# Kernel optimization log

Measured on AMD Instinct MI355X. Metric: run time of the kernel, lower is better.

The kernel has to match this reference:

```python
import jax, jax.numpy as jnp
import numpy as np

N_NODES = 100000
N_EDGES = 1600000
DIMS = [1, 20, 40, 60, 80, 100]  # int(k/5*qubo_size) for qubo_size=100


def setup_inputs() -> dict:
    key = jax.random.key(0)
    ks = jax.random.split(key, 16)
    inp = {
        "x": jax.random.normal(ks[0], (N_NODES, 1), dtype=jnp.float32),
        "edge_index": jax.random.randint(ks[1], (2, N_EDGES), 0, N_NODES, dtype=jnp.int64),
        "edge_weights": jax.random.uniform(ks[2], (N_EDGES,), dtype=jnp.float32),
    }
    for i in range(5):
        fan_in, fan_out = DIMS[i], DIMS[i + 1]
        scale = (2.0 / (fan_in + fan_out)) ** 0.5  # glorot-ish
        inp[f"W{i+1}"] = jax.random.normal(ks[3 + 2 * i], (fan_in, fan_out), dtype=jnp.float32) * scale
        inp[f"b{i+1}"] = jnp.zeros((fan_out,), dtype=jnp.float32)
    return inp


def reference(x, edge_index, edge_weights, W1, b1, W2, b2, W3, b3, W4, b4, W5, b5):
    n = x.shape[0]
    src, dst = edge_index[0], edge_index[1]
    # GCN symmetric normalization with self loops (fill value 1.0)
    deg = jax.ops.segment_sum(edge_weights, dst, num_segments=n) + 1.0
    dinv = jnp.where(deg > 0, deg ** -0.5, 0.0)
    norm = dinv[src] * edge_weights * dinv[dst]  # [E]
    self_norm = dinv * dinv                      # [N], self-loop weight 1

    def gcn_layer(h, W, b):
        h = h @ W  # [N, out]
        agg = jax.ops.segment_sum(h[src] * norm[:, None], dst, num_segments=n)
        agg = agg + h * self_norm[:, None]
        return agg + b

    for W, b in ((W1, b1), (W2, b2), (W3, b3), (W4, b4), (W5, b5)):
        x = gcn_layer(x, W, b)
    return jax.nn.relu(x)
```

## Files before the change

kernel.cpp:

```cpp
#include <hip/hip_runtime.h>


#define TBB 1024
#define TBK 512
#define BN 256
#define NBLK 256
#define CAP 4864
#define EPB 7
#define MAGIC 0x13572468

__device__ __forceinline__ void chains_block(
    const float* __restrict__ W1, const float* __restrict__ b1,
    const float* __restrict__ W2, const float* __restrict__ b2,
    const float* __restrict__ W3, const float* __restrict__ b3,
    const float* __restrict__ W4, const float* __restrict__ b4,
    const float* __restrict__ W5, float* __restrict__ coef,
    int* lflag, float (*A)[112], float (*Bm)[112]) {
    int t = threadIdx.x;
    if (t < 20) { A[0][t] = W1[t]; A[1][t] = b1[t]; }
    __syncthreads();
    if (t < 40) {
        for (int c = 0; c < 2; ++c) {
            float acc = 0.f;
            for (int k = 0; k < 20; ++k) acc += A[c][k] * W2[k * 40 + t];
            Bm[c][t] = acc;
        }
        Bm[2][t] = b2[t];
    }
    __syncthreads();
    if (t < 60) {
        for (int c = 0; c < 3; ++c) {
            float acc = 0.f;
            for (int k = 0; k < 40; ++k) acc += Bm[c][k] * W3[k * 60 + t];
            A[c][t] = acc;
        }
        A[3][t] = b3[t];
    }
    __syncthreads();
    if (t < 80) {
        for (int c = 0; c < 4; ++c) {
            float acc = 0.f;
            for (int k = 0; k < 60; ++k) acc += A[c][k] * W4[k * 80 + t];
            Bm[c][t] = acc;
        }
        Bm[4][t] = b4[t];
    }
    __syncthreads();
    if (t < 100) {
        int nz = 0;
        for (int c = 0; c < 5; ++c) {
            float acc = 0.f;
            for (int k = 0; k < 80; ++k) acc += Bm[c][k] * W5[k * 100 + t];
            coef[c * 100 + t] = acc;
            if (c > 0 && acc != 0.0f) nz = 1;
        }
        if (nz) atomicOr(lflag, 1);
    }
}

__global__ __launch_bounds__(TBB) void k_build(const int* __restrict__ src,
                                               const int* __restrict__ dst,
                                               const float* __restrict__ w,
                                               int* __restrict__ gcur,
                                               int* __restrict__ ready,
                                               int2* __restrict__ payload,
                                               const float* __restrict__ W1, const float* __restrict__ b1,
                                               const float* __restrict__ W2, const float* __restrict__ b2,
                                               const float* __restrict__ W3, const float* __restrict__ b3,
                                               const float* __restrict__ W4, const float* __restrict__ b4,
                                               const float* __restrict__ W5, float* __restrict__ coef,
                                               int* __restrict__ uflag,
                                               int E, int B, int chunk) {
    __shared__ int lcnt[512];
    __shared__ int lrnk[512];
    __shared__ int goff[512];
    __shared__ float chain_scratch[10][112];
    int blk = blockIdx.x, tid = threadIdx.x;
    if (blk == NBLK) {
        if (tid == 0) lcnt[0] = 0;
        __syncthreads();
        chains_block(W1, b1, W2, b2, W3, b3, W4, b4, W5, coef, &lcnt[0],
                     &chain_scratch[0], &chain_scratch[5]);
        __syncthreads();
        if (tid == 0) uflag[0] = lcnt[0] ? 0 : 1;
        return;
    }
    if (blk == 0) {
        for (int j2 = tid; j2 < B; j2 += TBB) gcur[j2] = 0;
        __syncthreads();
        if (tid == 0)
            __hip_atomic_store(ready, MAGIC, __ATOMIC_RELEASE, __HIP_MEMORY_SCOPE_AGENT);
    }
    if (tid < 512) { lcnt[tid] = 0; lrnk[tid] = 0; }
    __syncthreads();
    int e0 = blk * chunk, e1 = min(E, e0 + chunk);
    int es[EPB], ed[EPB]; float ew[EPB]; int ne = 0;
    for (int i = e0 + tid; i < e1; i += TBB) {
        es[ne] = src[i]; ed[ne] = dst[i]; ew[ne] = w[i]; ++ne;
    }
    for (int k = 0; k < ne; ++k) atomicAdd(&lcnt[ed[k] >> 8], 1);
    __syncthreads();
    if (blk != 0) {
        if (tid == 0) {
            while (__hip_atomic_load(ready, __ATOMIC_ACQUIRE, __HIP_MEMORY_SCOPE_AGENT) != MAGIC)
                __builtin_amdgcn_s_sleep(1);
        }
        __syncthreads();
    }
    if (tid < 512) {
        int c = lcnt[tid];
        if (c > 0) goff[tid] = atomicAdd(&gcur[tid], c);
    }
    __syncthreads();
    for (int k = 0; k < ne; ++k) {
        int j = ed[k] >> 8;
        int r = atomicAdd(&lrnk[j], 1);
        int slot = goff[j] + r;
        if (slot < CAP)
            payload[(size_t)j * CAP + slot] =
                make_int2(es[k] | ((ed[k] & 255) << 17), __float_as_int(ew[k]));
    }
}

__global__ __launch_bounds__(TBK) void k_bstats(const int* __restrict__ gcur,
                                                const int2* __restrict__ payload,
                                                const float* __restrict__ x,
                                                float* __restrict__ dinv,
                                                float* __restrict__ selfn,
                                                float* __restrict__ qx0,
                                                float* __restrict__ qy0, int n) {
    __shared__ float wdeg[BN];
    int j = blockIdx.x;
    int tid = threadIdx.x;
    if (tid < BN) wdeg[tid] = 0.f;
    __syncthreads();
    int len = min(gcur[j], CAP);
    const int2* row = payload + (size_t)j * CAP;
    const int4* row4 = (const int4*)row;
    int len2 = len >> 1;
    for (int i = tid; i < len2; i += TBK) {
        int4 p = row4[i];
        atomicAdd(&wdeg[(p.x >> 17) & 255], __int_as_float(p.y));
        atomicAdd(&wdeg[(p.z >> 17) & 255], __int_as_float(p.w));
    }
    if (tid == 0 && (len & 1)) {
        int2 p = row[len - 1];
        atomicAdd(&wdeg[(p.x >> 17) & 255], __int_as_float(p.y));
    }
    __syncthreads();
    if (tid < BN) {
        int v = j * BN + tid;
        if (v < n) {
            float di = rsqrtf(wdeg[tid] + 1.0f);
            dinv[v] = di;
            selfn[v] = di * di;
            qx0[v] = di * x[v];
            qy0[v] = di;
        }
    }
}

__global__ __launch_bounds__(TBK) void k_mid(const int* __restrict__ gcur,
                                             const int2* __restrict__ payload,
                                             const float* __restrict__ qxin,
                                             const float* __restrict__ qyin,
                                             const float* __restrict__ selfn,
                                             const int* __restrict__ uflag,
                                             float* __restrict__ qxout,
                                             float* __restrict__ qyout, int n) {
    __shared__ float sacc_x[BN];
    __shared__ float sacc_y[BN];
    int j = blockIdx.x;
    int tid = threadIdx.x;
    if (tid < BN) { sacc_x[tid] = 0.f; sacc_y[tid] = 0.f; }
    __syncthreads();
    const int skipy = uflag[0];
    int len = min(gcur[j], CAP);
    const int2* row = payload + (size_t)j * CAP;
    const int4* row4 = (const int4*)row;
    int len2 = len >> 1;
    for (int i = tid; i < len2; i += TBK) {
        int4 p = row4[i];
        int s1 = p.x & 0x1FFFF, s2 = p.z & 0x1FFFF;
        int ld1 = (p.x >> 17) & 255, ld2 = (p.z >> 17) & 255;
        float w1 = __int_as_float(p.y), w2 = __int_as_float(p.w);
        if (skipy) {
            float qx1 = qxin[s1], qx2 = qxin[s2];
            atomicAdd(&sacc_x[ld1], w1 * qx1);
            atomicAdd(&sacc_x[ld2], w2 * qx2);
        } else {
            float qx1 = qxin[s1], qy1 = qyin[s1];
            float qx2 = qxin[s2], qy2 = qyin[s2];
            atomicAdd(&sacc_x[ld1], w1 * qx1);
            atomicAdd(&sacc_y[ld1], w1 * qy1);
            atomicAdd(&sacc_x[ld2], w2 * qx2);
            atomicAdd(&sacc_y[ld2], w2 * qy2);
        }
    }
    if (tid == 0 && (len & 1)) {
        int2 p = row[len - 1];
        int s = p.x & 0x1FFFF, ld = (p.x >> 17) & 255;
        float wv = __int_as_float(p.y);
        atomicAdd(&sacc_x[ld], wv * qxin[s]);
        if (!skipy) atomicAdd(&sacc_y[ld], wv * qyin[s]);
    }
    __syncthreads();
    if (tid < BN) {
        int v = j * BN + tid;
        if (v < n) {
            float sf = selfn[v];
            qxout[v] = sf * (sacc_x[tid] + qxin[v]);
            if (!skipy) qyout[v] = sf * (sacc_y[tid] + qyin[v]);
        }
    }
}

__global__ __launch_bounds__(TBK) void k_last(const int* __restrict__ gcur,
                                              const int2* __restrict__ payload,
                                              const float* __restrict__ qx4,
                                              const float* __restrict__ qy1,
                                              const float* __restrict__ qy2,
                                              const float* __restrict__ qy3,
                                              const float* __restrict__ qy4,
                                              const float* __restrict__ dinv,
                                              const int* __restrict__ uflag,
                                              const float* __restrict__ coef,
                                              const float* __restrict__ b5,
                                              float4* __restrict__ out, int n) {
    __shared__ float sacc_x[BN];
    __shared__ float scoef[500];
    __shared__ float sb5[100];
    __shared__ float snode[BN * 5];
    int j = blockIdx.x;
    int tid = threadIdx.x;
    if (tid < BN) sacc_x[tid] = 0.f;
    for (int i = tid; i < 500; i += TBK) scoef[i] = coef[i];
    for (int i = tid; i < 100; i += TBK) sb5[i] = b5[i];
    __syncthreads();
    const int skipy = uflag[0];
    int len = min(gcur[j], CAP);
    const int2* row = payload + (size_t)j * CAP;
    const int4* row4 = (const int4*)row;
    int len2 = len >> 1;
    for (int i = tid; i < len2; i += TBK) {
        int4 p = row4[i];
        float qx1 = qx4[p.x & 0x1FFFF];
        float qx2 = qx4[p.z & 0x1FFFF];
        atomicAdd(&sacc_x[(p.x >> 17) & 255], __int_as_float(p.y) * qx1);
        atomicAdd(&sacc_x[(p.z >> 17) & 255], __int_as_float(p.w) * qx2);
    }
    if (tid == 0 && (len & 1)) {
        int2 p = row[len - 1];
        atomicAdd(&sacc_x[(p.x >> 17) & 255], __int_as_float(p.y) * qx4[p.x & 0x1FFFF]);
    }
    __syncthreads();
    if (tid < BN) {
        int v = j * BN + tid;
        if (v < n) {
            float dv = dinv[v];
            float inv = 1.0f / dv;
            snode[tid * 5 + 0] = dv * (sacc_x[tid] + qx4[v]);
            snode[tid * 5 + 1] = skipy ? 0.f : qy4[v] * inv;
            snode[tid * 5 + 2] = skipy ? 0.f : qy3[v] * inv;
            snode[tid * 5 + 3] = skipy ? 0.f : qy2[v] * inv;
            snode[tid * 5 + 4] = skipy ? 0.f : qy1[v] * inv;
        }
    }
    __syncthreads();
    int base_v = j * BN;
    int nv = min(BN, n - base_v);
    int total4 = nv * 25;
    for (int q = tid; q < total4; q += TBK) {
        int lv = q / 25;
        int col4 = q - lv * 25;
        int c0 = col4 * 4;
        float a5 = snode[lv * 5 + 0], u4 = snode[lv * 5 + 1], u3 = snode[lv * 5 + 2],
              u2 = snode[lv * 5 + 3], u1 = snode[lv * 5 + 4];
        float4 r;
        float* rp = (float*)&r;
#pragma unroll
        for (int kk = 0; kk < 4; ++kk) {
            int c = c0 + kk;
            rp[kk] = fmaxf(sb5[c] + a5 * scoef[c] + u4 * scoef[100 + c] + u3 * scoef[200 + c]
                           + u2 * scoef[300 + c] + u1 * scoef[400 + c], 0.f);
        }
        out[(size_t)(base_v + lv) * 25 + col4] = r;
    }
}


extern "C" void kernel_launch(void* const* d_in, const int* in_sizes, int n_in,
                              void* d_out, int out_size, void* d_ws, size_t ws_size,
                              hipStream_t stream) {
    const float* x  = (const float*)d_in[0];
    const int*   ei = (const int*)d_in[1];
    const float* w  = (const float*)d_in[2];
    const float* W1 = (const float*)d_in[3];  const float* b1 = (const float*)d_in[4];
    const float* W2 = (const float*)d_in[5];  const float* b2 = (const float*)d_in[6];
    const float* W3 = (const float*)d_in[7];  const float* b3 = (const float*)d_in[8];
    const float* W4 = (const float*)d_in[9];  const float* b4 = (const float*)d_in[10];
    const float* W5 = (const float*)d_in[11]; const float* b5 = (const float*)d_in[12];

    const int n = in_sizes[0];
    const int E = in_sizes[2];
    const int* src = ei;
    const int* dst = ei + E;

    const int B = (n + BN - 1) / BN;
    const int chunk = (E + NBLK - 1) / NBLK;

    char* ws = (char*)d_ws;
    size_t off = 0;
    auto alloc = [&](size_t bytes) -> void* {
        void* p = ws + off;
        off += (bytes + 255) & ~(size_t)255;
        return p;
    };
    int*   gcur    = (int*)alloc((size_t)B * 4);
    int*   ready   = (int*)alloc(256);
    int*   uflag   = (int*)alloc(256);
    float* dinv    = (float*)alloc((size_t)n * 4);
    float* selfn   = (float*)alloc((size_t)n * 4);
    float* coef    = (float*)alloc(512 * 4);
    int2*  payload = (int2*)alloc((size_t)B * CAP * 8);
    float* qx[5];
    float* qy[5];
    for (int i = 0; i < 5; ++i) qx[i] = (float*)alloc((size_t)n * 4);
    for (int i = 0; i < 5; ++i) qy[i] = (float*)alloc((size_t)n * 4);

    k_build<<<NBLK + 1, TBB, 0, stream>>>(src, dst, w, gcur, ready, payload,
                                          W1, b1, W2, b2, W3, b3, W4, b4, W5, coef,
                                          uflag, E, B, chunk);
    k_bstats<<<B, TBK, 0, stream>>>(gcur, payload, x, dinv, selfn, qx[0], qy[0], n);

    for (int k = 1; k < 5; ++k)
        k_mid<<<B, TBK, 0, stream>>>(gcur, payload, qx[k - 1], qy[k - 1], selfn, uflag,
                                     qx[k], qy[k], n);
    k_last<<<B, TBK, 0, stream>>>(gcur, payload, qx[4], qy[1], qy[2], qy[3], qy[4],
                                  dinv, uflag, coef, b5, (float4*)d_out, n);
}
```

Before: 206.1 us.

## Fuse all stages into one persistent kernel with grid barriers and LDS-cached bucket rows

Merges the build, degree-stats, four middle propagation passes and final output pass into a single kernel of B=391 blocks (512 threads each), synchronised by atomic grid barriers. Each block caches its destination bucket's payload row in shared memory once and reuses it across all six passes. dinv and selfn now stay in shared memory instead of global arrays. This removes six kernel launches and the repeated global payload reads. In exchange, correctness depends on all 391 blocks being co-resident: a software grid barrier without cooperative launch can deadlock if they are not. The large shared-memory footprint (about 39 KB for the row alone) also limits occupancy.

```diff
diff --git a/kernel.cpp b/kernel.cpp
--- a/kernel.cpp
+++ b/kernel.cpp
@@ -1,12 +1,10 @@
 #include <hip/hip_runtime.h>
 
 
-#define TBB 1024
 #define TBK 512
 #define BN 256
-#define NBLK 256
 #define CAP 4864
-#define EPB 7
+#define EPB 8
 #define MAGIC 0x13572468
 
 __device__ __forceinline__ void chains_block(
@@ -58,213 +56,203 @@
     }
 }
 
-__global__ __launch_bounds__(TBB) void k_build(const int* __restrict__ src,
-                                               const int* __restrict__ dst,
-                                               const float* __restrict__ w,
-                                               int* __restrict__ gcur,
-                                               int* __restrict__ ready,
-                                               int2* __restrict__ payload,
-                                               const float* __restrict__ W1, const float* __restrict__ b1,
-                                               const float* __restrict__ W2, const float* __restrict__ b2,
-                                               const float* __restrict__ W3, const float* __restrict__ b3,
-                                               const float* __restrict__ W4, const float* __restrict__ b4,
-                                               const float* __restrict__ W5, float* __restrict__ coef,
-                                               int* __restrict__ uflag,
-                                               int E, int B, int chunk) {
-    __shared__ int lcnt[512];
-    __shared__ int lrnk[512];
-    __shared__ int goff[512];
-    __shared__ float chain_scratch[10][112];
-    int blk = blockIdx.x, tid = threadIdx.x;
-    if (blk == NBLK) {
-        if (tid == 0) lcnt[0] = 0;
-        __syncthreads();
-        chains_block(W1, b1, W2, b2, W3, b3, W4, b4, W5, coef, &lcnt[0],
-                     &chain_scratch[0], &chain_scratch[5]);
-        __syncthreads();
-        if (tid == 0) uflag[0] = lcnt[0] ? 0 : 1;
-        return;
-    }
-    if (blk == 0) {
-        for (int j2 = tid; j2 < B; j2 += TBB) gcur[j2] = 0;
-        __syncthreads();
-        if (tid == 0)
-            __hip_atomic_store(ready, MAGIC, __ATOMIC_RELEASE, __HIP_MEMORY_SCOPE_AGENT);
-    }
-    if (tid < 512) { lcnt[tid] = 0; lrnk[tid] = 0; }
-    __syncthreads();
-    int e0 = blk * chunk, e1 = min(E, e0 + chunk);
-    int es[EPB], ed[EPB]; float ew[EPB]; int ne = 0;
-    for (int i = e0 + tid; i < e1; i += TBB) {
-        es[ne] = src[i]; ed[ne] = dst[i]; ew[ne] = w[i]; ++ne;
-    }
-    for (int k = 0; k < ne; ++k) atomicAdd(&lcnt[ed[k] >> 8], 1);
-    __syncthreads();
-    if (blk != 0) {
-        if (tid == 0) {
-            while (__hip_atomic_load(ready, __ATOMIC_ACQUIRE, __HIP_MEMORY_SCOPE_AGENT) != MAGIC)
-                __builtin_amdgcn_s_sleep(1);
-        }
-        __syncthreads();
-    }
-    if (tid < 512) {
-        int c = lcnt[tid];
-        if (c > 0) goff[tid] = atomicAdd(&gcur[tid], c);
-    }
-    __syncthreads();
-    for (int k = 0; k < ne; ++k) {
-        int j = ed[k] >> 8;
-        int r = atomicAdd(&lrnk[j], 1);
-        int slot = goff[j] + r;
-        if (slot < CAP)
-            payload[(size_t)j * CAP + slot] =
-                make_int2(es[k] | ((ed[k] & 255) << 17), __float_as_int(ew[k]));
-    }
-}
-
-__global__ __launch_bounds__(TBK) void k_bstats(const int* __restrict__ gcur,
-                                                const int2* __restrict__ payload,
-                                                const float* __restrict__ x,
-                                                float* __restrict__ dinv,
-                                                float* __restrict__ selfn,
-                                                float* __restrict__ qx0,
-                                                float* __restrict__ qy0, int n) {
-    __shared__ float wdeg[BN];
-    int j = blockIdx.x;
+__device__ __forceinline__ void gbar(int* bar, int target) {
+    __syncthreads();
+    if (threadIdx.x == 0) {
+        __hip_atomic_fetch_add(bar, 1, __ATOMIC_RELEASE, __HIP_MEMORY_SCOPE_AGENT);
+        while (__hip_atomic_load(bar, __ATOMIC_RELAXED, __HIP_MEMORY_SCOPE_AGENT) < target)
+            __builtin_amdgcn_s_sleep(2);
+        __builtin_amdgcn_fence(__ATOMIC_ACQUIRE, "agent");
+    }
+    __syncthreads();
+}
+
+__device__ __forceinline__ void midpass(const int4* srow, int len,
+                                        const float* qxin, const float* qyin,
+                                        float* qxout, float* qyout,
+                                        float* sacc_x, float* sacc_y,
+                                        const float* sselfn, int skipy, int n) {
     int tid = threadIdx.x;
-    if (tid < BN) wdeg[tid] = 0.f;
-    __syncthreads();
-    int len = min(gcur[j], CAP);
-    const int2* row = payload + (size_t)j * CAP;
-    const int4* row4 = (const int4*)row;
+    if (tid < BN) { sacc_x[tid] = 0.f; sacc_y[tid] = 0.f; }
+    __syncthreads();
     int len2 = len >> 1;
     for (int i = tid; i < len2; i += TBK) {
-        int4 p = row4[i];
-        atomicAdd(&wdeg[(p.x >> 17) & 255], __int_as_float(p.y));
-        atomicAdd(&wdeg[(p.z >> 17) & 255], __int_as_float(p.w));
-    }
-    if (tid == 0 && (len & 1)) {
-        int2 p = row[len - 1];
-        atomicAdd(&wdeg[(p.x >> 17) & 255], __int_as_float(p.y));
-    }
-    __syncthreads();
-    if (tid < BN) {
-        int v = j * BN + tid;
-        if (v < n) {
-            float di = rsqrtf(wdeg[tid] + 1.0f);
-            dinv[v] = di;
-            selfn[v] = di * di;
-            qx0[v] = di * x[v];
-            qy0[v] = di;
-        }
-    }
-}
-
-__global__ __launch_bounds__(TBK) void k_mid(const int* __restrict__ gcur,
-                                             const int2* __restrict__ payload,
-                                             const float* __restrict__ qxin,
-                                             const float* __restrict__ qyin,
-                                             const float* __restrict__ selfn,
-                                             const int* __restrict__ uflag,
-                                             float* __restrict__ qxout,
-                                             float* __restrict__ qyout, int n) {
-    __shared__ float sacc_x[BN];
-    __shared__ float sacc_y[BN];
-    int j = blockIdx.x;
-    int tid = threadIdx.x;
-    if (tid < BN) { sacc_x[tid] = 0.f; sacc_y[tid] = 0.f; }
-    __syncthreads();
-    const int skipy = uflag[0];
-    int len = min(gcur[j], CAP);
-    const int2* row = payload + (size_t)j * CAP;
-    const int4* row4 = (const int4*)row;
-    int len2 = len >> 1;
-    for (int i = tid; i < len2; i += TBK) {
-        int4 p = row4[i];
+        int4 p = srow[i];
         int s1 = p.x & 0x1FFFF, s2 = p.z & 0x1FFFF;
         int ld1 = (p.x >> 17) & 255, ld2 = (p.z >> 17) & 255;
         float w1 = __int_as_float(p.y), w2 = __int_as_float(p.w);
         if (skipy) {
-            float qx1 = qxin[s1], qx2 = qxin[s2];
-            atomicAdd(&sacc_x[ld1], w1 * qx1);
-            atomicAdd(&sacc_x[ld2], w2 * qx2);
+            atomicAdd(&sacc_x[ld1], w1 * qxin[s1]);
+            atomicAdd(&sacc_x[ld2], w2 * qxin[s2]);
         } else {
-            float qx1 = qxin[s1], qy1 = qyin[s1];
-            float qx2 = qxin[s2], qy2 = qyin[s2];
-            atomicAdd(&sacc_x[ld1], w1 * qx1);
-            atomicAdd(&sacc_y[ld1], w1 * qy1);
-            atomicAdd(&sacc_x[ld2], w2 * qx2);
-            atomicAdd(&sacc_y[ld2], w2 * qy2);
+            float qxa = qxin[s1], qya = qyin[s1];
+            float qxb = qxin[s2], qyb = qyin[s2];
+            atomicAdd(&sacc_x[ld1], w1 * qxa);
+            atomicAdd(&sacc_y[ld1], w1 * qya);
+            atomicAdd(&sacc_x[ld2], w2 * qxb);
+            atomicAdd(&sacc_y[ld2], w2 * qyb);
         }
     }
     if (tid == 0 && (len & 1)) {
-        int2 p = row[len - 1];
+        int4 p = srow[len2];
         int s = p.x & 0x1FFFF, ld = (p.x >> 17) & 255;
         float wv = __int_as_float(p.y);
         atomicAdd(&sacc_x[ld], wv * qxin[s]);
         if (!skipy) atomicAdd(&sacc_y[ld], wv * qyin[s]);
     }
     __syncthreads();
-    if (tid < BN) {
-        int v = j * BN + tid;
-        if (v < n) {
-            float sf = selfn[v];
-            qxout[v] = sf * (sacc_x[tid] + qxin[v]);
-            if (!skipy) qyout[v] = sf * (sacc_y[tid] + qyin[v]);
-        }
-    }
-}
-
-__global__ __launch_bounds__(TBK) void k_last(const int* __restrict__ gcur,
-                                              const int2* __restrict__ payload,
-                                              const float* __restrict__ qx4,
-                                              const float* __restrict__ qy1,
-                                              const float* __restrict__ qy2,
-                                              const float* __restrict__ qy3,
-                                              const float* __restrict__ qy4,
-                                              const float* __restrict__ dinv,
-                                              const int* __restrict__ uflag,
-                                              const float* __restrict__ coef,
-                                              const float* __restrict__ b5,
-                                              float4* __restrict__ out, int n) {
+    int v = blockIdx.x * BN + tid;
+    if (tid < BN && v < n) {
+        float sf = sselfn[tid];
+        qxout[v] = sf * (sacc_x[tid] + qxin[v]);
+        if (!skipy) qyout[v] = sf * (sacc_y[tid] + qyin[v]);
+    }
+}
+
+__global__ __launch_bounds__(TBK, 4) void k_all(
+    const int* __restrict__ src, const int* __restrict__ dst,
+    const float* __restrict__ w, const float* __restrict__ x,
+    const float* __restrict__ W1, const float* __restrict__ b1,
+    const float* __restrict__ W2, const float* __restrict__ b2,
+    const float* __restrict__ W3, const float* __restrict__ b3,
+    const float* __restrict__ W4, const float* __restrict__ b4,
+    const float* __restrict__ W5, const float* __restrict__ b5,
+    int* gcur, int* ready, int* bar, int* uflag, float* coef,
+    int2* payload,
+    float* qx0, float* qx1, float* qx2, float* qx3, float* qx4,
+    float* qy0, float* qy1, float* qy2, float* qy3, float* qy4,
+    float4* out, int n, int E, int B, int chunk) {
+    __shared__ int lcnt[512];
+    __shared__ int lrnk[512];
+    __shared__ int goff[512];
+    __shared__ int4 srow[CAP / 2];
     __shared__ float sacc_x[BN];
+    __shared__ float sacc_y[BN];
+    __shared__ float sdinv[BN];
+    __shared__ float sselfn[BN];
     __shared__ float scoef[500];
     __shared__ float sb5[100];
     __shared__ float snode[BN * 5];
-    int j = blockIdx.x;
-    int tid = threadIdx.x;
+
+    int j = blockIdx.x, tid = threadIdx.x;
+
+    lcnt[tid] = 0; lrnk[tid] = 0;
+    __syncthreads();
+    int e0 = j * chunk, e1 = min(E, e0 + chunk);
+    int es[EPB], ed[EPB]; float ew[EPB];
+#pragma unroll
+    for (int k = 0; k < EPB; ++k) {
+        int i = e0 + tid + k * TBK;
+        if (i < e1) { es[k] = src[i]; ed[k] = dst[i]; ew[k] = w[i]; }
+        else ed[k] = -1;
+    }
+#pragma unroll
+    for (int k = 0; k < EPB; ++k)
+        if (ed[k] >= 0) atomicAdd(&lcnt[ed[k] >> 8], 1);
+    __syncthreads();
+    if (j == 0) {
+        for (int q = tid; q < B; q += TBK) gcur[q] = 0;
+        if (tid == 0) bar[0] = 0;
+        __syncthreads();
+        if (tid == 0)
+            __hip_atomic_store(ready, MAGIC, __ATOMIC_RELEASE, __HIP_MEMORY_SCOPE_AGENT);
+    } else {
+        if (tid == 0) {
+            while (__hip_atomic_load(ready, __ATOMIC_RELAXED, __HIP_MEMORY_SCOPE_AGENT) != MAGIC)
+                __builtin_amdgcn_s_sleep(2);
+            __builtin_amdgcn_fence(__ATOMIC_ACQUIRE, "agent");
+        }
+        __syncthreads();
+    }
+    {
+        int c = lcnt[tid];
+        if (c > 0) goff[tid] = atomicAdd(&gcur[tid], c);
+    }
+    __syncthreads();
+#pragma unroll
+    for (int k = 0; k < EPB; ++k) {
+        if (ed[k] >= 0) {
+            int b = ed[k] >> 8;
+            int r = atomicAdd(&lrnk[b], 1);
+            int slot = goff[b] + r;
+            if (slot < CAP)
+                payload[(size_t)b * CAP + slot] =
+                    make_int2(es[k] | ((ed[k] & 255) << 17), __float_as_int(ew[k]));
+        }
+    }
+    gbar(bar, B);
+
+    int len = min(gcur[j], CAP);
+    int len2 = len >> 1;
+    int nq4 = (len + 1) >> 1;
+    const int4* row4g = (const int4*)(payload + (size_t)j * CAP);
+    for (int i = tid; i < nq4; i += TBK) srow[i] = row4g[i];
     if (tid < BN) sacc_x[tid] = 0.f;
+    __syncthreads();
+    for (int i = tid; i < len2; i += TBK) {
+        int4 p = srow[i];
+        atomicAdd(&sacc_x[(p.x >> 17) & 255], __int_as_float(p.y));
+        atomicAdd(&sacc_x[(p.z >> 17) & 255], __int_as_float(p.w));
+    }
+    if (tid == 0 && (len & 1)) {
+        int4 p = srow[len2];
+        atomicAdd(&sacc_x[(p.x >> 17) & 255], __int_as_float(p.y));
+    }
+    __syncthreads();
+    int v = j * BN + tid;
+    if (tid < BN && v < n) {
+        float di = rsqrtf(sacc_x[tid] + 1.0f);
+        sdinv[tid] = di;
+        sselfn[tid] = di * di;
+        qx0[v] = di * x[v];
+        qy0[v] = di;
+    }
+    if (j == 0) {
+        float (*A)[112]  = (float (*)[112])snode;
+        float (*Bm)[112] = (float (*)[112])(snode + 5 * 112);
+        if (tid == 0) lcnt[0] = 0;
+        __syncthreads();
+        chains_block(W1, b1, W2, b2, W3, b3, W4, b4, W5, coef, &lcnt[0], A, Bm);
+        __syncthreads();
+        if (tid == 0) uflag[0] = lcnt[0] ? 0 : 1;
+    }
+    gbar(bar, 2 * B);
+
+    const int skipy = uflag[0];
     for (int i = tid; i < 500; i += TBK) scoef[i] = coef[i];
     for (int i = tid; i < 100; i += TBK) sb5[i] = b5[i];
-    __syncthreads();
-    const int skipy = uflag[0];
-    int len = min(gcur[j], CAP);
-    const int2* row = payload + (size_t)j * CAP;
-    const int4* row4 = (const int4*)row;
-    int len2 = len >> 1;
+
+    midpass(srow, len, qx0, qy0, qx1, qy1, sacc_x, sacc_y, sselfn, skipy, n);
+    gbar(bar, 3 * B);
+    midpass(srow, len, qx1, qy1, qx2, qy2, sacc_x, sacc_y, sselfn, skipy, n);
+    gbar(bar, 4 * B);
+    midpass(srow, len, qx2, qy2, qx3, qy3, sacc_x, sacc_y, sselfn, skipy, n);
+    gbar(bar, 5 * B);
+    midpass(srow, len, qx3, qy3, qx4, qy4, sacc_x, sacc_y, sselfn, skipy, n);
+    gbar(bar, 6 * B);
+
+    if (tid < BN) sacc_x[tid] = 0.f;
+    __syncthreads();
     for (int i = tid; i < len2; i += TBK) {
-        int4 p = row4[i];
-        float qx1 = qx4[p.x & 0x1FFFF];
-        float qx2 = qx4[p.z & 0x1FFFF];
-        atomicAdd(&sacc_x[(p.x >> 17) & 255], __int_as_float(p.y) * qx1);
-        atomicAdd(&sacc_x[(p.z >> 17) & 255], __int_as_float(p.w) * qx2);
+        int4 p = srow[i];
+        float q1 = qx4[p.x & 0x1FFFF];
+        float q2 = qx4[p.z & 0x1FFFF];
+        atomicAdd(&sacc_x[(p.x >> 17) & 255], __int_as_float(p.y) * q1);
+        atomicAdd(&sacc_x[(p.z >> 17) & 255], __int_as_float(p.w) * q2);
     }
     if (tid == 0 && (len & 1)) {
-        int2 p = row[len - 1];
+        int4 p = srow[len2];
         atomicAdd(&sacc_x[(p.x >> 17) & 255], __int_as_float(p.y) * qx4[p.x & 0x1FFFF]);
     }
     __syncthreads();
-    if (tid < BN) {
-        int v = j * BN + tid;
-        if (v < n) {
-            float dv = dinv[v];
-            float inv = 1.0f / dv;
-            snode[tid * 5 + 0] = dv * (sacc_x[tid] + qx4[v]);
-            snode[tid * 5 + 1] = skipy ? 0.f : qy4[v] * inv;
-            snode[tid * 5 + 2] = skipy ? 0.f : qy3[v] * inv;
-            snode[tid * 5 + 3] = skipy ? 0.f : qy2[v] * inv;
-            snode[tid * 5 + 4] = skipy ? 0.f : qy1[v] * inv;
-        }
+    if (tid < BN && v < n) {
+        float dv = sdinv[tid];
+        float inv = 1.0f / dv;
+        snode[tid * 5 + 0] = dv * (sacc_x[tid] + qx4[v]);
+        snode[tid * 5 + 1] = skipy ? 0.f : qy4[v] * inv;
+        snode[tid * 5 + 2] = skipy ? 0.f : qy3[v] * inv;
+        snode[tid * 5 + 3] = skipy ? 0.f : qy2[v] * inv;
+        snode[tid * 5 + 4] = skipy ? 0.f : qy1[v] * inv;
     }
     __syncthreads();
     int base_v = j * BN;
@@ -307,7 +295,7 @@
     const int* dst = ei + E;
 
     const int B = (n + BN - 1) / BN;
-    const int chunk = (E + NBLK - 1) / NBLK;
+    const int chunk = (E + B - 1) / B;
 
     char* ws = (char*)d_ws;
     size_t off = 0;
@@ -318,9 +306,8 @@
     };
     int*   gcur    = (int*)alloc((size_t)B * 4);
     int*   ready   = (int*)alloc(256);
+    int*   bar     = (int*)alloc(256);
     int*   uflag   = (int*)alloc(256);
-    float* dinv    = (float*)alloc((size_t)n * 4);
-    float* selfn   = (float*)alloc((size_t)n * 4);
     float* coef    = (float*)alloc(512 * 4);
     int2*  payload = (int2*)alloc((size_t)B * CAP * 8);
     float* qx[5];
@@ -328,14 +315,10 @@
     for (int i = 0; i < 5; ++i) qx[i] = (float*)alloc((size_t)n * 4);
     for (int i = 0; i < 5; ++i) qy[i] = (float*)alloc((size_t)n * 4);
 
-    k_build<<<NBLK + 1, TBB, 0, stream>>>(src, dst, w, gcur, ready, payload,
-                                          W1, b1, W2, b2, W3, b3, W4, b4, W5, coef,
-                                          uflag, E, B, chunk);
-    k_bstats<<<B, TBK, 0, stream>>>(gcur, payload, x, dinv, selfn, qx[0], qy[0], n);
-
-    for (int k = 1; k < 5; ++k)
-        k_mid<<<B, TBK, 0, stream>>>(gcur, payload, qx[k - 1], qy[k - 1], selfn, uflag,
-                                     qx[k], qy[k], n);
-    k_last<<<B, TBK, 0, stream>>>(gcur, payload, qx[4], qy[1], qy[2], qy[3], qy[4],
-                                  dinv, uflag, coef, b5, (float4*)d_out, n);
-}
+    k_all<<<B, TBK, 0, stream>>>(src, dst, w, x,
+                                 W1, b1, W2, b2, W3, b3, W4, b4, W5, b5,
+                                 gcur, ready, bar, uflag, coef, payload,
+                                 qx[0], qx[1], qx[2], qx[3], qx[4],
+                                 qy[0], qy[1], qy[2], qy[3], qy[4],
+                                 (float4*)d_out, n, E, B, chunk);
+}
```

New measurement: 419.7 us. 104% more time.

## Interleave qx/qy as float2, drop bias skip flag, fully unroll edge loops

Applied to the files above, without the earlier changes.

Stores the two propagated per-node vectors together as float2, so each edge needs one 8-byte gather for both components. It also removes the runtime flag that skipped the y-path when the bias chain coefficients were all zero. The aggregation loops in k_mid and k_last become five fixed register-held slots per thread, loading every payload entry before the dependent gathers and LDS atomics to raise memory-level parallelism, and the build kernel's edge loop is fully unrolled. The trade-off is that the y gathers and LDS atomics now always run, even when the biases are zero, which doubles shared-memory atomic traffic in that case.

```diff
diff --git a/kernel.cpp b/kernel.cpp
--- a/kernel.cpp
+++ b/kernel.cpp
@@ -7,6 +7,7 @@
 #define NBLK 256
 #define CAP 4864
 #define EPB 7
+#define NSLOT 5
 #define MAGIC 0x13572468
 
 __device__ __forceinline__ void chains_block(
@@ -15,7 +16,7 @@
     const float* __restrict__ W3, const float* __restrict__ b3,
     const float* __restrict__ W4, const float* __restrict__ b4,
     const float* __restrict__ W5, float* __restrict__ coef,
-    int* lflag, float (*A)[112], float (*Bm)[112]) {
+    float (*A)[112], float (*Bm)[112]) {
     int t = threadIdx.x;
     if (t < 20) { A[0][t] = W1[t]; A[1][t] = b1[t]; }
     __syncthreads();
@@ -47,14 +48,11 @@
     }
     __syncthreads();
     if (t < 100) {
-        int nz = 0;
         for (int c = 0; c < 5; ++c) {
             float acc = 0.f;
             for (int k = 0; k < 80; ++k) acc += Bm[c][k] * W5[k * 100 + t];
             coef[c * 100 + t] = acc;
-            if (c > 0 && acc != 0.0f) nz = 1;
-        }
-        if (nz) atomicOr(lflag, 1);
+        }
     }
 }
 
@@ -69,7 +67,6 @@
                                                const float* __restrict__ W3, const float* __restrict__ b3,
                                                const float* __restrict__ W4, const float* __restrict__ b4,
                                                const float* __restrict__ W5, float* __restrict__ coef,
-                                               int* __restrict__ uflag,
                                                int E, int B, int chunk) {
     __shared__ int lcnt[512];
     __shared__ int lrnk[512];
@@ -77,12 +74,8 @@
     __shared__ float chain_scratch[10][112];
     int blk = blockIdx.x, tid = threadIdx.x;
     if (blk == NBLK) {
-        if (tid == 0) lcnt[0] = 0;
-        __syncthreads();
-        chains_block(W1, b1, W2, b2, W3, b3, W4, b4, W5, coef, &lcnt[0],
+        chains_block(W1, b1, W2, b2, W3, b3, W4, b4, W5, coef,
                      &chain_scratch[0], &chain_scratch[5]);
-        __syncthreads();
-        if (tid == 0) uflag[0] = lcnt[0] ? 0 : 1;
         return;
     }
     if (blk == 0) {
@@ -94,11 +87,16 @@
     if (tid < 512) { lcnt[tid] = 0; lrnk[tid] = 0; }
     __syncthreads();
     int e0 = blk * chunk, e1 = min(E, e0 + chunk);
-    int es[EPB], ed[EPB]; float ew[EPB]; int ne = 0;
-    for (int i = e0 + tid; i < e1; i += TBB) {
-        es[ne] = src[i]; ed[ne] = dst[i]; ew[ne] = w[i]; ++ne;
-    }
-    for (int k = 0; k < ne; ++k) atomicAdd(&lcnt[ed[k] >> 8], 1);
+    int es[EPB], ed[EPB]; float ew[EPB];
+#pragma unroll
+    for (int k = 0; k < EPB; ++k) {
+        int i = e0 + tid + k * TBB;
+        if (i < e1) { es[k] = src[i]; ed[k] = dst[i]; ew[k] = w[i]; }
+        else ed[k] = -1;
+    }
+#pragma unroll
+    for (int k = 0; k < EPB; ++k)
+        if (ed[k] >= 0) atomicAdd(&lcnt[ed[k] >> 8], 1);
     __syncthreads();
     if (blk != 0) {
         if (tid == 0) {
@@ -112,13 +110,16 @@
         if (c > 0) goff[tid] = atomicAdd(&gcur[tid], c);
     }
     __syncthreads();
-    for (int k = 0; k < ne; ++k) {
-        int j = ed[k] >> 8;
-        int r = atomicAdd(&lrnk[j], 1);
-        int slot = goff[j] + r;
-        if (slot < CAP)
-            payload[(size_t)j * CAP + slot] =
-                make_int2(es[k] | ((ed[k] & 255) << 17), __float_as_int(ew[k]));
+#pragma unroll
+    for (int k = 0; k < EPB; ++k) {
+        if (ed[k] >= 0) {
+            int b = ed[k] >> 8;
+            int r = atomicAdd(&lrnk[b], 1);
+            int slot = goff[b] + r;
+            if (slot < CAP)
+                payload[(size_t)b * CAP + slot] =
+                    make_int2(es[k] | ((ed[k] & 255) << 17), __float_as_int(ew[k]));
+        }
     }
 }
 
@@ -127,8 +128,7 @@
                                                 const float* __restrict__ x,
                                                 float* __restrict__ dinv,
                                                 float* __restrict__ selfn,
-                                                float* __restrict__ qx0,
-                                                float* __restrict__ qy0, int n) {
+                                                float2* __restrict__ qxy0, int n) {
     __shared__ float wdeg[BN];
     int j = blockIdx.x;
     int tid = threadIdx.x;
@@ -154,104 +154,137 @@
             float di = rsqrtf(wdeg[tid] + 1.0f);
             dinv[v] = di;
             selfn[v] = di * di;
-            qx0[v] = di * x[v];
-            qy0[v] = di;
+            qxy0[v] = make_float2(di * x[v], di);
         }
     }
 }
 
 __global__ __launch_bounds__(TBK) void k_mid(const int* __restrict__ gcur,
                                              const int2* __restrict__ payload,
-                                             const float* __restrict__ qxin,
-                                             const float* __restrict__ qyin,
+                                             const float2* __restrict__ qin,
                                              const float* __restrict__ selfn,
-                                             const int* __restrict__ uflag,
-                                             float* __restrict__ qxout,
-                                             float* __restrict__ qyout, int n) {
-    __shared__ float sacc_x[BN];
-    __shared__ float sacc_y[BN];
+                                             float2* __restrict__ qout, int n) {
+    __shared__ float sx[BN];
+    __shared__ float sy[BN];
     int j = blockIdx.x;
     int tid = threadIdx.x;
-    if (tid < BN) { sacc_x[tid] = 0.f; sacc_y[tid] = 0.f; }
-    __syncthreads();
-    const int skipy = uflag[0];
+    if (tid < BN) { sx[tid] = 0.f; sy[tid] = 0.f; }
+    __syncthreads();
     int len = min(gcur[j], CAP);
     const int2* row = payload + (size_t)j * CAP;
     const int4* row4 = (const int4*)row;
     int len2 = len >> 1;
-    for (int i = tid; i < len2; i += TBK) {
-        int4 p = row4[i];
-        int s1 = p.x & 0x1FFFF, s2 = p.z & 0x1FFFF;
-        int ld1 = (p.x >> 17) & 255, ld2 = (p.z >> 17) & 255;
-        float w1 = __int_as_float(p.y), w2 = __int_as_float(p.w);
-        if (skipy) {
-            float qx1 = qxin[s1], qx2 = qxin[s2];
-            atomicAdd(&sacc_x[ld1], w1 * qx1);
-            atomicAdd(&sacc_x[ld2], w2 * qx2);
-        } else {
-            float qx1 = qxin[s1], qy1 = qyin[s1];
-            float qx2 = qxin[s2], qy2 = qyin[s2];
-            atomicAdd(&sacc_x[ld1], w1 * qx1);
-            atomicAdd(&sacc_y[ld1], w1 * qy1);
-            atomicAdd(&sacc_x[ld2], w2 * qx2);
-            atomicAdd(&sacc_y[ld2], w2 * qy2);
-        }
-    }
+    int4 p0, p1, p2, p3, p4;
+    {
+        int i0 = tid, i1 = tid + TBK, i2 = tid + 2 * TBK, i3 = tid + 3 * TBK,
+            i4 = tid + 4 * TBK;
+        p0 = (i0 < len2) ? row4[i0] : make_int4(0, 0, 0, 0);
+        p1 = (i1 < len2) ? row4[i1] : make_int4(0, 0, 0, 0);
+        p2 = (i2 < len2) ? row4[i2] : make_int4(0, 0, 0, 0);
+        p3 = (i3 < len2) ? row4[i3] : make_int4(0, 0, 0, 0);
+        p4 = (i4 < len2) ? row4[i4] : make_int4(0, 0, 0, 0);
+    }
+    float2 a0 = qin[p0.x & 0x1FFFF], b0 = qin[p0.z & 0x1FFFF];
+    float2 a1 = qin[p1.x & 0x1FFFF], b1 = qin[p1.z & 0x1FFFF];
+    float2 a2 = qin[p2.x & 0x1FFFF], b2 = qin[p2.z & 0x1FFFF];
+    float2 a3 = qin[p3.x & 0x1FFFF], b3 = qin[p3.z & 0x1FFFF];
+    float2 a4 = qin[p4.x & 0x1FFFF], b4 = qin[p4.z & 0x1FFFF];
+    float w0a = __int_as_float(p0.y), w0b = __int_as_float(p0.w);
+    float w1a = __int_as_float(p1.y), w1b = __int_as_float(p1.w);
+    float w2a = __int_as_float(p2.y), w2b = __int_as_float(p2.w);
+    float w3a = __int_as_float(p3.y), w3b = __int_as_float(p3.w);
+    float w4a = __int_as_float(p4.y), w4b = __int_as_float(p4.w);
+    atomicAdd(&sx[(p0.x >> 17) & 255], w0a * a0.x);
+    atomicAdd(&sy[(p0.x >> 17) & 255], w0a * a0.y);
+    atomicAdd(&sx[(p0.z >> 17) & 255], w0b * b0.x);
+    atomicAdd(&sy[(p0.z >> 17) & 255], w0b * b0.y);
+    atomicAdd(&sx[(p1.x >> 17) & 255], w1a * a1.x);
+    atomicAdd(&sy[(p1.x >> 17) & 255], w1a * a1.y);
+    atomicAdd(&sx[(p1.z >> 17) & 255], w1b * b1.x);
+    atomicAdd(&sy[(p1.z >> 17) & 255], w1b * b1.y);
+    atomicAdd(&sx[(p2.x >> 17) & 255], w2a * a2.x);
+    atomicAdd(&sy[(p2.x >> 17) & 255], w2a * a2.y);
+    atomicAdd(&sx[(p2.z >> 17) & 255], w2b * b2.x);
+    atomicAdd(&sy[(p2.z >> 17) & 255], w2b * b2.y);
+    atomicAdd(&sx[(p3.x >> 17) & 255], w3a * a3.x);
+    atomicAdd(&sy[(p3.x >> 17) & 255], w3a * a3.y);
+    atomicAdd(&sx[(p3.z >> 17) & 255], w3b * b3.x);
+    atomicAdd(&sy[(p3.z >> 17) & 255], w3b * b3.y);
+    atomicAdd(&sx[(p4.x >> 17) & 255], w4a * a4.x);
+    atomicAdd(&sy[(p4.x >> 17) & 255], w4a * a4.y);
+    atomicAdd(&sx[(p4.z >> 17) & 255], w4b * b4.x);
+    atomicAdd(&sy[(p4.z >> 17) & 255], w4b * b4.y);
     if (tid == 0 && (len & 1)) {
         int2 p = row[len - 1];
-        int s = p.x & 0x1FFFF, ld = (p.x >> 17) & 255;
+        float2 g = qin[p.x & 0x1FFFF];
         float wv = __int_as_float(p.y);
-        atomicAdd(&sacc_x[ld], wv * qxin[s]);
-        if (!skipy) atomicAdd(&sacc_y[ld], wv * qyin[s]);
+        atomicAdd(&sx[(p.x >> 17) & 255], wv * g.x);
+        atomicAdd(&sy[(p.x >> 17) & 255], wv * g.y);
     }
     __syncthreads();
     if (tid < BN) {
         int v = j * BN + tid;
         if (v < n) {
             float sf = selfn[v];
-            qxout[v] = sf * (sacc_x[tid] + qxin[v]);
-            if (!skipy) qyout[v] = sf * (sacc_y[tid] + qyin[v]);
+            float2 qv = qin[v];
+            qout[v] = make_float2(sf * (sx[tid] + qv.x), sf * (sy[tid] + qv.y));
         }
     }
 }
 
 __global__ __launch_bounds__(TBK) void k_last(const int* __restrict__ gcur,
                                               const int2* __restrict__ payload,
-                                              const float* __restrict__ qx4,
-                                              const float* __restrict__ qy1,
-                                              const float* __restrict__ qy2,
-                                              const float* __restrict__ qy3,
-                                              const float* __restrict__ qy4,
+                                              const float2* __restrict__ qxy4,
+                                              const float2* __restrict__ qxy1,
+                                              const float2* __restrict__ qxy2,
+                                              const float2* __restrict__ qxy3,
                                               const float* __restrict__ dinv,
-                                              const int* __restrict__ uflag,
                                               const float* __restrict__ coef,
                                               const float* __restrict__ b5,
                                               float4* __restrict__ out, int n) {
-    __shared__ float sacc_x[BN];
+    __shared__ float sx[BN];
     __shared__ float scoef[500];
     __shared__ float sb5[100];
     __shared__ float snode[BN * 5];
     int j = blockIdx.x;
     int tid = threadIdx.x;
-    if (tid < BN) sacc_x[tid] = 0.f;
+    if (tid < BN) sx[tid] = 0.f;
     for (int i = tid; i < 500; i += TBK) scoef[i] = coef[i];
     for (int i = tid; i < 100; i += TBK) sb5[i] = b5[i];
     __syncthreads();
-    const int skipy = uflag[0];
     int len = min(gcur[j], CAP);
     const int2* row = payload + (size_t)j * CAP;
     const int4* row4 = (const int4*)row;
     int len2 = len >> 1;
-    for (int i = tid; i < len2; i += TBK) {
-        int4 p = row4[i];
-        float qx1 = qx4[p.x & 0x1FFFF];
-        float qx2 = qx4[p.z & 0x1FFFF];
-        atomicAdd(&sacc_x[(p.x >> 17) & 255], __int_as_float(p.y) * qx1);
-        atomicAdd(&sacc_x[(p.z >> 17) & 255], __int_as_float(p.w) * qx2);
+    {
+        int4 p0, p1, p2, p3, p4;
+        int i0 = tid, i1 = tid + TBK, i2 = tid + 2 * TBK, i3 = tid + 3 * TBK,
+            i4 = tid + 4 * TBK;
+        p0 = (i0 < len2) ? row4[i0] : make_int4(0, 0, 0, 0);
+        p1 = (i1 < len2) ? row4[i1] : make_int4(0, 0, 0, 0);
+        p2 = (i2 < len2) ? row4[i2] : make_int4(0, 0, 0, 0);
+        p3 = (i3 < len2) ? row4[i3] : make_int4(0, 0, 0, 0);
+        p4 = (i4 < len2) ? row4[i4] : make_int4(0, 0, 0, 0);
+        float ga0 = qxy4[p0.x & 0x1FFFF].x, gb0 = qxy4[p0.z & 0x1FFFF].x;
+        float ga1 = qxy4[p1.x & 0x1FFFF].x, gb1 = qxy4[p1.z & 0x1FFFF].x;
+        float ga2 = qxy4[p2.x & 0x1FFFF].x, gb2 = qxy4[p2.z & 0x1FFFF].x;
+        float ga3 = qxy4[p3.x & 0x1FFFF].x, gb3 = qxy4[p3.z & 0x1FFFF].x;
+        float ga4 = qxy4[p4.x & 0x1FFFF].x, gb4 = qxy4[p4.z & 0x1FFFF].x;
+        atomicAdd(&sx[(p0.x >> 17) & 255], __int_as_float(p0.y) * ga0);
+        atomicAdd(&sx[(p0.z >> 17) & 255], __int_as_float(p0.w) * gb0);
+        atomicAdd(&sx[(p1.x >> 17) & 255], __int_as_float(p1.y) * ga1);
+        atomicAdd(&sx[(p1.z >> 17) & 255], __int_as_float(p1.w) * gb1);
+        atomicAdd(&sx[(p2.x >> 17) & 255], __int_as_float(p2.y) * ga2);
+        atomicAdd(&sx[(p2.z >> 17) & 255], __int_as_float(p2.w) * gb2);
+        atomicAdd(&sx[(p3.x >> 17) & 255], __int_as_float(p3.y) * ga3);
+        atomicAdd(&sx[(p3.z >> 17) & 255], __int_as_float(p3.w) * gb3);
+        atomicAdd(&sx[(p4.x >> 17) & 255], __int_as_float(p4.y) * ga4);
+        atomicAdd(&sx[(p4.z >> 17) & 255], __int_as_float(p4.w) * gb4);
     }
     if (tid == 0 && (len & 1)) {
         int2 p = row[len - 1];
-        atomicAdd(&sacc_x[(p.x >> 17) & 255], __int_as_float(p.y) * qx4[p.x & 0x1FFFF]);
+        atomicAdd(&sx[(p.x >> 17) & 255],
+                  __int_as_float(p.y) * qxy4[p.x & 0x1FFFF].x);
     }
     __syncthreads();
     if (tid < BN) {
@@ -259,11 +292,11 @@
         if (v < n) {
             float dv = dinv[v];
             float inv = 1.0f / dv;
-            snode[tid * 5 + 0] = dv * (sacc_x[tid] + qx4[v]);
-            snode[tid * 5 + 1] = skipy ? 0.f : qy4[v] * inv;
-            snode[tid * 5 + 2] = skipy ? 0.f : qy3[v] * inv;
-            snode[tid * 5 + 3] = skipy ? 0.f : qy2[v] * inv;
-            snode[tid * 5 + 4] = skipy ? 0.f : qy1[v] * inv;
+            snode[tid * 5 + 0] = dv * (sx[tid] + qxy4[v].x);
+            snode[tid * 5 + 1] = qxy4[v].y * inv;
+            snode[tid * 5 + 2] = qxy3[v].y * inv;
+            snode[tid * 5 + 3] = qxy2[v].y * inv;
+            snode[tid * 5 + 4] = qxy1[v].y * inv;
         }
     }
     __syncthreads();
@@ -316,26 +349,22 @@
         off += (bytes + 255) & ~(size_t)255;
         return p;
     };
-    int*   gcur    = (int*)alloc((size_t)B * 4);
-    int*   ready   = (int*)alloc(256);
-    int*   uflag   = (int*)alloc(256);
-    float* dinv    = (float*)alloc((size_t)n * 4);
-    float* selfn   = (float*)alloc((size_t)n * 4);
-    float* coef    = (float*)alloc(512 * 4);
-    int2*  payload = (int2*)alloc((size_t)B * CAP * 8);
-    float* qx[5];
-    float* qy[5];
-    for (int i = 0; i < 5; ++i) qx[i] = (float*)alloc((size_t)n * 4);
-    for (int i = 0; i < 5; ++i) qy[i] = (float*)alloc((size_t)n * 4);
+    int*    gcur    = (int*)alloc((size_t)B * 4);
+    int*    ready   = (int*)alloc(256);
+    float*  dinv    = (float*)alloc((size_t)n * 4);
+    float*  selfn   = (float*)alloc((size_t)n * 4);
+    float*  coef    = (float*)alloc(512 * 4);
+    int2*   payload = (int2*)alloc((size_t)B * CAP * 8);
+    float2* qxy[5];
+    for (int i = 0; i < 5; ++i) qxy[i] = (float2*)alloc((size_t)n * 8);
 
     k_build<<<NBLK + 1, TBB, 0, stream>>>(src, dst, w, gcur, ready, payload,
                                           W1, b1, W2, b2, W3, b3, W4, b4, W5, coef,
-                                          uflag, E, B, chunk);
-    k_bstats<<<B, TBK, 0, stream>>>(gcur, payload, x, dinv, selfn, qx[0], qy[0], n);
+                                          E, B, chunk);
+    k_bstats<<<B, TBK, 0, stream>>>(gcur, payload, x, dinv, selfn, qxy[0], n);
 
     for (int k = 1; k < 5; ++k)
-        k_mid<<<B, TBK, 0, stream>>>(gcur, payload, qx[k - 1], qy[k - 1], selfn, uflag,
-                                     qx[k], qy[k], n);
-    k_last<<<B, TBK, 0, stream>>>(gcur, payload, qx[4], qy[1], qy[2], qy[3], qy[4],
-                                  dinv, uflag, coef, b5, (float4*)d_out, n);
-}
+        k_mid<<<B, TBK, 0, stream>>>(gcur, payload, qxy[k - 1], selfn, qxy[k], n);
+    k_last<<<B, TBK, 0, stream>>>(gcur, payload, qxy[4], qxy[1], qxy[2], qxy[3],
+                                  dinv, coef, b5, (float4*)d_out, n);
+}
```

Result: slower. 289.5 us (+40.4%).
